# Optimization experiments

Hardware: AMD Instinct MI355X
Metric: run time of the kernel (lower is better)

Reference implementation:

```python
import jax, jax.numpy as jnp
import numpy as np

N = 200000   # active voxels
K = 27       # 3x3x3 kernel volume
CIN = 32
COUT = 64


def setup_inputs() -> dict:
    key = jax.random.key(0)
    k1, k2, k3, k4 = jax.random.split(key, 4)
    features = jax.random.normal(k1, (N, CIN), dtype=jnp.float32)
    # kernel map: for each kernel offset k and output voxel n, index of the
    # contributing input voxel (or masked out if that neighbor is inactive)
    neighbor_map = jax.random.randint(k2, (K, N), 0, N, dtype=jnp.int32)
    neighbor_mask = jax.random.randint(k3, (K, N), 0, 2) > 0
    std = 1.0 / float(np.sqrt(CIN * K))  # matches reset_parameters
    kernel = jax.random.uniform(k4, (K, CIN, COUT), dtype=jnp.float32,
                                minval=-std, maxval=std)
    return {"features": features, "neighbor_map": neighbor_map,
            "neighbor_mask": neighbor_mask, "kernel": kernel}


def reference(features, neighbor_map, neighbor_mask, kernel):
    # Sparse conv3d as gather -> per-offset matmul -> accumulate.
    # scan over the K=27 kernel offsets keeps peak memory at one gathered
    # [N, CIN] buffer instead of materializing [K, N, CIN].
    n_out = features.shape[0]
    cout = kernel.shape[-1]

    def body(acc, inp):
        nm_k, mask_k, w_k = inp  # [N], [N], [CIN, COUT]
        g = features[nm_k] * mask_k[:, None].astype(features.dtype)  # gather [N, CIN]
        return acc + g @ w_k, None

    init = jnp.zeros((n_out, cout), dtype=features.dtype)
    out, _ = jax.lax.scan(body, init, (neighbor_map, neighbor_mask, kernel))
    return out
```

## Files before the change

kernel.cpp:

```cpp
#include <hip/hip_runtime.h>

#define CIN   32
#define COUT  64
#define K_OFF 27

typedef __attribute__((ext_vector_type(8))) short bf16x8;
typedef __attribute__((ext_vector_type(4))) float f32x4;

__device__ inline unsigned short f2bf_rne(float f) {
    union { float f; unsigned int u; } v; v.f = f;
    unsigned int u = v.u;
    u = (u + 0x7fffu + ((u >> 16) & 1u)) >> 16;
    return (unsigned short)u;
}

__global__ __launch_bounds__(256) void detect_mask(
    const unsigned char* __restrict__ mask, int nbytes, int* __restrict__ flag) {
    __shared__ int wany[4];
    int found = 0;
    for (int i = threadIdx.x; i < nbytes; i += 256)
        if ((i & 3) && mask[i]) found = 1;
    unsigned long long b = __ballot(found);
    if ((threadIdx.x & 63) == 0) wany[threadIdx.x >> 6] = b ? 1 : 0;
    __syncthreads();
    if (threadIdx.x == 0) *flag = wany[0] | wany[1] | wany[2] | wany[3];
}

__global__ __launch_bounds__(256) void prep_kernel(
    const float* __restrict__ feat, const int* __restrict__ nmap,
    const unsigned char* __restrict__ mask8, const int* __restrict__ mask32,
    const float* __restrict__ wk,
    unsigned short* __restrict__ featb, int* __restrict__ midx,
    unsigned short* __restrict__ wt2,
    int n, int Bf, int Bm, const int* __restrict__ flag)
{
    const int gid = blockIdx.x;
    if (gid < Bf) {
        const int base = (gid * 256 + threadIdx.x) * 8;
        if (base < n * CIN) {
            float4 a = *(const float4*)(feat + base);
            float4 b = *(const float4*)(feat + base + 4);
            bf16x8 v;
            v[0] = (short)f2bf_rne(a.x); v[1] = (short)f2bf_rne(a.y);
            v[2] = (short)f2bf_rne(a.z); v[3] = (short)f2bf_rne(a.w);
            v[4] = (short)f2bf_rne(b.x); v[5] = (short)f2bf_rne(b.y);
            v[6] = (short)f2bf_rne(b.z); v[7] = (short)f2bf_rne(b.w);
            *(bf16x8*)(featb + base) = v;
        }
    } else if (gid < Bf + Bm) {
        const int t = (gid - Bf) * 256 + threadIdx.x;
        int i = t * 4;
        const int total = K_OFF * n;
        const int is_b8 = *flag;
        if (i + 3 < total) {
            int4 nm = *(const int4*)(nmap + i);
            int m0, m1, m2, m3;
            if (is_b8) {
                uchar4 mb = *(const uchar4*)(mask8 + i);
                m0 = mb.x; m1 = mb.y; m2 = mb.z; m3 = mb.w;
            } else {
                int4 mm = *(const int4*)(mask32 + i);
                m0 = mm.x; m1 = mm.y; m2 = mm.z; m3 = mm.w;
            }
            int4 r;
            r.x = m0 ? nm.x : -1; r.y = m1 ? nm.y : -1;
            r.z = m2 ? nm.z : -1; r.w = m3 ? nm.w : -1;
            *(int4*)(midx + i) = r;
        } else {
            for (; i < total; ++i) {
                int m = is_b8 ? (int)mask8[i] : mask32[i];
                midx[i] = m ? nmap[i] : -1;
            }
        }
    } else {
        const int t = (gid - Bf - Bm) * 256 + threadIdx.x;
        if (t < K_OFF * 4 * 64) {
            const int lane = t & 63, ct = (t >> 6) & 3, k = t >> 8;
            const int lrow = lane & 15, q = lane >> 4;
            const int col = ct * 16 + lrow;
            bf16x8 v;
            #pragma unroll
            for (int j = 0; j < 8; ++j)
                v[j] = (short)f2bf_rne(wk[(k * CIN + q * 8 + j) * COUT + col]);
            *(bf16x8*)(wt2 + t * 8) = v;
        }
    }
}

__global__ __attribute__((amdgpu_waves_per_eu(3, 4))) __launch_bounds__(256)
void conv_mfma7(
    const unsigned short* __restrict__ featb,
    const int*            __restrict__ midx,
    const unsigned short* __restrict__ wt2,
    float* __restrict__ out, int n)
{
    const int tid  = threadIdx.x;
    const int wave = tid >> 6;
    const int lane = tid & 63;
    const int lrow = lane & 15;
    const int q    = lane >> 4;
    const int n0   = blockIdx.x * 128 + wave * 32;

    const int  row0 = n0 + lrow, row1 = n0 + 16 + lrow;
    const bool vr0 = row0 < n, vr1 = row1 < n;

    auto load_mi = [&](int k, int rt) -> int {
        const int  r = rt ? row1 : row0;
        const bool v = rt ? vr1 : vr0;
        if (!v) return -1;
        return midx[k * n + r];
    };
    auto gather = [&](int mi) -> bf16x8 {
        bf16x8 z = {0, 0, 0, 0, 0, 0, 0, 0};
        if (mi >= 0) z = *(const bf16x8*)(featb + (size_t)mi * CIN + q * 8);
        return z;
    };
    auto loadB = [&](int k, bf16x8* dst) {
        const unsigned short* p = wt2 + ((k * 4) << 9) + lane * 8;
        #pragma unroll
        for (int ct = 0; ct < 4; ++ct) dst[ct] = *(const bf16x8*)(p + (ct << 9));
    };

    int    mi_buf[2][2];
    bf16x8 a_buf[3][2];
    bf16x8 B_buf[2][4];
    f32x4  acc[2][4] = {};

    {
        int t0 = load_mi(0, 0), t1 = load_mi(0, 1);
        int u0 = load_mi(1, 0), u1 = load_mi(1, 1);
        mi_buf[0][0] = load_mi(2, 0);
        mi_buf[0][1] = load_mi(2, 1);
        a_buf[0][0] = gather(t0); a_buf[0][1] = gather(t1);
        a_buf[1][0] = gather(u0); a_buf[1][1] = gather(u1);
        loadB(0, B_buf[0]);
    }

    #pragma unroll
    for (int k = 0; k < K_OFF; ++k) {
        if (k + 3 < K_OFF) {
            mi_buf[(k + 1) & 1][0] = load_mi(k + 3, 0);
            mi_buf[(k + 1) & 1][1] = load_mi(k + 3, 1);
        }
        if (k + 2 < K_OFF) {
            a_buf[(k + 2) % 3][0] = gather(mi_buf[k & 1][0]);
            a_buf[(k + 2) % 3][1] = gather(mi_buf[k & 1][1]);
        }
        if (k + 1 < K_OFF) loadB(k + 1, B_buf[(k + 1) & 1]);

        const int s = k % 3, bs = k & 1;
        #pragma unroll
        for (int ct = 0; ct < 4; ++ct) {
            acc[0][ct] = __builtin_amdgcn_mfma_f32_16x16x32_bf16(
                a_buf[s][0], B_buf[bs][ct], acc[0][ct], 0, 0, 0);
            acc[1][ct] = __builtin_amdgcn_mfma_f32_16x16x32_bf16(
                a_buf[s][1], B_buf[bs][ct], acc[1][ct], 0, 0, 0);
        }
    }

    #pragma unroll
    for (int rt = 0; rt < 2; ++rt)
        #pragma unroll
        for (int ct = 0; ct < 4; ++ct)
            #pragma unroll
            for (int r = 0; r < 4; ++r) {
                const int row = n0 + rt * 16 + q * 4 + r;
                if (row < n) out[(size_t)row * COUT + ct * 16 + lrow] = acc[rt][ct][r];
            }
}

#define BN 64
__global__ __launch_bounds__(256) void sparse_conv_fp32(
    const float* __restrict__ feat, const int* __restrict__ nmap,
    const unsigned char* __restrict__ mask8, const int* __restrict__ mask32,
    const float* __restrict__ wk, float* __restrict__ out,
    int n, const int* __restrict__ flag)
{
    __shared__ float A[CIN][BN];
    __shared__ float W[CIN][COUT];
    const int tid = threadIdx.x;
    const int n0 = blockIdx.x * BN;
    const int is_b8 = *flag;
    const int r0 = (tid >> 4) * 4, c0 = (tid & 15) * 4;
    const int grow = tid >> 2, gpart = tid & 3;
    float acc[4][4] = {};
    for (int k = 0; k < K_OFF; ++k) {
        {
            const int base = tid * 8;
            const float* wsrc = wk + (size_t)k * (CIN * COUT) + base;
            float4 w0 = ((const float4*)wsrc)[0];
            float4 w1 = ((const float4*)wsrc)[1];
            *(float4*)&W[base >> 6][base & 63] = w0;
            *(float4*)&W[base >> 6][(base & 63) + 4] = w1;
        }
        {
            const int gn = n0 + grow;
            float4 f0 = make_float4(0.f, 0.f, 0.f, 0.f), f1 = f0;
            if (gn < n) {
                const int idx = k * n + gn;
                const int m = is_b8 ? (int)mask8[idx] : mask32[idx];
                if (m) {
                    const float* fsrc = feat + (size_t)nmap[idx] * CIN + gpart * 8;
                    f0 = ((const float4*)fsrc)[0];
                    f1 = ((const float4*)fsrc)[1];
                }
            }
            const int cb = gpart * 8;
            A[cb+0][grow]=f0.x; A[cb+1][grow]=f0.y; A[cb+2][grow]=f0.z; A[cb+3][grow]=f0.w;
            A[cb+4][grow]=f1.x; A[cb+5][grow]=f1.y; A[cb+6][grow]=f1.z; A[cb+7][grow]=f1.w;
        }
        __syncthreads();
        #pragma unroll
        for (int c = 0; c < CIN; ++c) {
            const float4 a = *(const float4*)&A[c][r0];
            const float4 w = *(const float4*)&W[c][c0];
            acc[0][0]+=a.x*w.x; acc[0][1]+=a.x*w.y; acc[0][2]+=a.x*w.z; acc[0][3]+=a.x*w.w;
            acc[1][0]+=a.y*w.x; acc[1][1]+=a.y*w.y; acc[1][2]+=a.y*w.z; acc[1][3]+=a.y*w.w;
            acc[2][0]+=a.z*w.x; acc[2][1]+=a.z*w.y; acc[2][2]+=a.z*w.z; acc[2][3]+=a.z*w.w;
            acc[3][0]+=a.w*w.x; acc[3][1]+=a.w*w.y; acc[3][2]+=a.w*w.z; acc[3][3]+=a.w*w.w;
        }
        __syncthreads();
    }
    #pragma unroll
    for (int i = 0; i < 4; ++i) {
        const int orow = n0 + r0 + i;
        if (orow < n)
            *(float4*)&out[(size_t)orow * COUT + c0] =
                make_float4(acc[i][0], acc[i][1], acc[i][2], acc[i][3]);
    }
}

static inline size_t align16(size_t x) { return (x + 15) & ~(size_t)15; }

extern "C" void kernel_launch(void* const* d_in, const int* in_sizes, int n_in,
                              void* d_out, int out_size, void* d_ws, size_t ws_size,
                              hipStream_t stream) {
    const float*         feat = (const float*)d_in[0];
    const int*           nmap = (const int*)d_in[1];
    const unsigned char* m8   = (const unsigned char*)d_in[2];
    const int*           m32  = (const int*)d_in[2];
    const float*         wk   = (const float*)d_in[3];
    float*               out  = (float*)d_out;

    const int n = in_sizes[0] / CIN;
    int* flag = (int*)d_ws;

    const size_t feat_off   = 128;
    const size_t feat_bytes = (size_t)n * CIN * 2;
    const size_t midx_off   = align16(feat_off + feat_bytes);
    const size_t midx_bytes = (size_t)K_OFF * n * 4;
    const size_t wt2_off    = align16(midx_off + midx_bytes);
    const size_t wt2_bytes  = (size_t)K_OFF * 4 * 64 * 8 * 2;
    const size_t needed     = wt2_off + wt2_bytes;

    const int mask_elems = K_OFF * n;
    const int det_bytes  = mask_elems < 4096 ? mask_elems : 4096;
    detect_mask<<<1, 256, 0, stream>>>(m8, det_bytes, flag);

    if (ws_size >= needed) {
        unsigned short* featb = (unsigned short*)((char*)d_ws + feat_off);
        int*            midx  = (int*)((char*)d_ws + midx_off);
        unsigned short* wt2   = (unsigned short*)((char*)d_ws + wt2_off);
        const int Bf = (n * CIN / 8 + 255) / 256;
        const int Bm = ((K_OFF * n + 3) / 4 + 255) / 256;
        const int Bw = (K_OFF * 4 * 64 + 255) / 256;
        prep_kernel<<<Bf + Bm + Bw, 256, 0, stream>>>(
            feat, nmap, m8, m32, wk, featb, midx, wt2, n, Bf, Bm, flag);
        const int nblocks = (n + 127) / 128;
        conv_mfma7<<<nblocks, 256, 0, stream>>>(featb, midx, wt2, out, n);
    } else {
        const int nb = (n + BN - 1) / BN;
        sparse_conv_fp32<<<nb, 256, 0, stream>>>(feat, nmap, m8, m32, wk, out, n, flag);
    }
}
```

Measured before the change: 176.7 us.

## Gather features via async global-to-LDS loads with deeper manual vmcnt pipeline

Replaces register-destined feature gathers with global_load_lds asynchronous copies into a 4-slot shared-memory ring per wave. Prefetch depth goes up to three offsets ahead for gathers and four for index loads, with hand-tuned s_waitcnt vmcnt fences. Masked rows now read from a zeroed scratch row instead of a branch. The waves_per_eu hint is dropped. The intent is to free VGPRs and keep more gathers in flight to hide latency, at the cost of fragile manual wait counts and 32KB of LDS per block, which may limit occupancy.

```diff
diff --git a/kernel.cpp b/kernel.cpp
--- a/kernel.cpp
+++ b/kernel.cpp
@@ -6,6 +6,9 @@
 
 typedef __attribute__((ext_vector_type(8))) short bf16x8;
 typedef __attribute__((ext_vector_type(4))) float f32x4;
+
+#define FENCE_VM(N) asm volatile("s_waitcnt vmcnt(" #N ")" ::: "memory")
+#define PIN()       asm volatile("" ::: "memory")
 
 __device__ inline unsigned short f2bf_rne(float f) {
     union { float f; unsigned int u; } v; v.f = f;
@@ -14,8 +17,15 @@
     return (unsigned short)u;
 }
 
+__device__ inline void async_load16(const void* g, void* l) {
+    __builtin_amdgcn_global_load_lds(
+        (const __attribute__((address_space(1))) void*)g,
+        (__attribute__((address_space(3))) void*)l, 16, 0, 0);
+}
+
 __global__ __launch_bounds__(256) void detect_mask(
-    const unsigned char* __restrict__ mask, int nbytes, int* __restrict__ flag) {
+    const unsigned char* __restrict__ mask, int nbytes, int* __restrict__ flag,
+    float* __restrict__ zrow) {
     __shared__ int wany[4];
     int found = 0;
     for (int i = threadIdx.x; i < nbytes; i += 256)
@@ -24,6 +34,7 @@
     if ((threadIdx.x & 63) == 0) wany[threadIdx.x >> 6] = b ? 1 : 0;
     __syncthreads();
     if (threadIdx.x == 0) *flag = wany[0] | wany[1] | wany[2] | wany[3];
+    if (threadIdx.x < 16) zrow[threadIdx.x] = 0.0f;
 }
 
 __global__ __launch_bounds__(256) void prep_kernel(
@@ -87,13 +98,18 @@
     }
 }
 
-__global__ __attribute__((amdgpu_waves_per_eu(3, 4))) __launch_bounds__(256)
-void conv_mfma7(
+__global__ __launch_bounds__(256) void conv_mfma9(
     const unsigned short* __restrict__ featb,
     const int*            __restrict__ midx,
     const unsigned short* __restrict__ wt2,
+    const unsigned short* __restrict__ zrow,
     float* __restrict__ out, int n)
 {
+    __shared__ __attribute__((aligned(16))) unsigned short As0[4][2][512];
+    __shared__ __attribute__((aligned(16))) unsigned short As1[4][2][512];
+    __shared__ __attribute__((aligned(16))) unsigned short As2[4][2][512];
+    __shared__ __attribute__((aligned(16))) unsigned short As3[4][2][512];
+
     const int tid  = threadIdx.x;
     const int wave = tid >> 6;
     const int lane = tid & 63;
@@ -110,10 +126,16 @@
         if (!v) return -1;
         return midx[k * n + r];
     };
-    auto gather = [&](int mi) -> bf16x8 {
-        bf16x8 z = {0, 0, 0, 0, 0, 0, 0, 0};
-        if (mi >= 0) z = *(const bf16x8*)(featb + (size_t)mi * CIN + q * 8);
-        return z;
+    auto slotp = [&](int s, int rt) -> unsigned short* {
+        return s == 0 ? &As0[wave][rt][0]
+             : s == 1 ? &As1[wave][rt][0]
+             : s == 2 ? &As2[wave][rt][0]
+                      : &As3[wave][rt][0];
+    };
+    auto issue_gather = [&](int mi, unsigned short* ldsbase) {
+        const unsigned short* src =
+            (mi >= 0) ? featb + (size_t)mi * CIN + q * 8 : zrow;
+        async_load16(src, ldsbase);
     };
     auto loadB = [&](int k, bf16x8* dst) {
         const unsigned short* p = wt2 + ((k * 4) << 9) + lane * 8;
@@ -122,39 +144,58 @@
     };
 
     int    mi_buf[2][2];
-    bf16x8 a_buf[3][2];
     bf16x8 B_buf[2][4];
     f32x4  acc[2][4] = {};
 
     {
-        int t0 = load_mi(0, 0), t1 = load_mi(0, 1);
-        int u0 = load_mi(1, 0), u1 = load_mi(1, 1);
-        mi_buf[0][0] = load_mi(2, 0);
-        mi_buf[0][1] = load_mi(2, 1);
-        a_buf[0][0] = gather(t0); a_buf[0][1] = gather(t1);
-        a_buf[1][0] = gather(u0); a_buf[1][1] = gather(u1);
+        int p00 = load_mi(0, 0), p01 = load_mi(0, 1);
+        int p10 = load_mi(1, 0), p11 = load_mi(1, 1);
+        int p20 = load_mi(2, 0), p21 = load_mi(2, 1);
+        mi_buf[1][0] = load_mi(3, 0);
+        mi_buf[1][1] = load_mi(3, 1);
+        PIN();
+        issue_gather(p00, slotp(0, 0)); issue_gather(p01, slotp(0, 1));
+        PIN();
+        issue_gather(p10, slotp(1, 0)); issue_gather(p11, slotp(1, 1));
+        PIN();
+        issue_gather(p20, slotp(2, 0)); issue_gather(p21, slotp(2, 1));
+        PIN();
         loadB(0, B_buf[0]);
+        PIN();
     }
 
     #pragma unroll
     for (int k = 0; k < K_OFF; ++k) {
+        if      (k == 0)  FENCE_VM(8);
+        else if (k == 1)  FENCE_VM(14);
+        else if (k <= 23) FENCE_VM(20);
+        else if (k == 24) FENCE_VM(18);
+        else if (k == 25) FENCE_VM(14);
+        else              FENCE_VM(12);
+
+        bf16x8 a0 = *(const bf16x8*)(slotp(k & 3, 0) + lane * 8);
+        bf16x8 a1 = *(const bf16x8*)(slotp(k & 3, 1) + lane * 8);
+
+        if (k + 4 < K_OFF) {
+            mi_buf[k & 1][0] = load_mi(k + 4, 0);
+            mi_buf[k & 1][1] = load_mi(k + 4, 1);
+        }
+        PIN();
         if (k + 3 < K_OFF) {
-            mi_buf[(k + 1) & 1][0] = load_mi(k + 3, 0);
-            mi_buf[(k + 1) & 1][1] = load_mi(k + 3, 1);
-        }
-        if (k + 2 < K_OFF) {
-            a_buf[(k + 2) % 3][0] = gather(mi_buf[k & 1][0]);
-            a_buf[(k + 2) % 3][1] = gather(mi_buf[k & 1][1]);
-        }
+            issue_gather(mi_buf[(k + 1) & 1][0], slotp((k + 3) & 3, 0));
+            issue_gather(mi_buf[(k + 1) & 1][1], slotp((k + 3) & 3, 1));
+        }
+        PIN();
         if (k + 1 < K_OFF) loadB(k + 1, B_buf[(k + 1) & 1]);
-
-        const int s = k % 3, bs = k & 1;
+        PIN();
+
+        const int bs = k & 1;
         #pragma unroll
         for (int ct = 0; ct < 4; ++ct) {
             acc[0][ct] = __builtin_amdgcn_mfma_f32_16x16x32_bf16(
-                a_buf[s][0], B_buf[bs][ct], acc[0][ct], 0, 0, 0);
+                a0, B_buf[bs][ct], acc[0][ct], 0, 0, 0);
             acc[1][ct] = __builtin_amdgcn_mfma_f32_16x16x32_bf16(
-                a_buf[s][1], B_buf[bs][ct], acc[1][ct], 0, 0, 0);
+                a1, B_buf[bs][ct], acc[1][ct], 0, 0, 0);
         }
     }
 
@@ -244,6 +285,7 @@
 
     const int n = in_sizes[0] / CIN;
     int* flag = (int*)d_ws;
+    float* zrow = (float*)((char*)d_ws + 64);
 
     const size_t feat_off   = 128;
     const size_t feat_bytes = (size_t)n * CIN * 2;
@@ -255,7 +297,7 @@
 
     const int mask_elems = K_OFF * n;
     const int det_bytes  = mask_elems < 4096 ? mask_elems : 4096;
-    detect_mask<<<1, 256, 0, stream>>>(m8, det_bytes, flag);
+    detect_mask<<<1, 256, 0, stream>>>(m8, det_bytes, flag, zrow);
 
     if (ws_size >= needed) {
         unsigned short* featb = (unsigned short*)((char*)d_ws + feat_off);
@@ -267,7 +309,8 @@
         prep_kernel<<<Bf + Bm + Bw, 256, 0, stream>>>(
             feat, nmap, m8, m32, wk, featb, midx, wt2, n, Bf, Bm, flag);
         const int nblocks = (n + 127) / 128;
-        conv_mfma7<<<nblocks, 256, 0, stream>>>(featb, midx, wt2, out, n);
+        conv_mfma9<<<nblocks, 256, 0, stream>>>(
+            featb, midx, wt2, (const unsigned short*)zrow, out, n);
     } else {
         const int nb = (n + BN - 1) / BN;
         sparse_conv_fp32<<<nb, 256, 0, stream>>>(feat, nmap, m8, m32, wk, out, n, flag);
```

Result: no change. 178.0 us (+0.8%).
